# Optimization experiments

Measured on AMD Instinct MI355X. Metric: run time of the kernel, lower is better.

Reference implementation:

```python
import jax, jax.numpy as jnp
import numpy as np

GROUPS = 8
EPS = 1e-5


def group_norm(x, gamma, beta):
    b, c, h, w = x.shape
    xg = x.reshape(b, GROUPS, c // GROUPS, h, w)
    mu = jnp.mean(xg, axis=(2, 3, 4), keepdims=True)
    var = jnp.mean((xg - mu) ** 2, axis=(2, 3, 4), keepdims=True)
    xn = ((xg - mu) * jax.lax.rsqrt(var + EPS)).reshape(b, c, h, w)
    return xn * gamma[None, :, None, None] + beta[None, :, None, None]


def setup_inputs() -> dict:
    key = jax.random.key(0)
    ks = jax.random.split(key, 4)
    b, c, h, w = 4, 64, 64, 64
    x = jax.random.normal(ks[0], (b, c, h, w), dtype=jnp.float32)
    gamma = jnp.ones((c,), dtype=jnp.float32)
    beta = jnp.zeros((c,), dtype=jnp.float32)
    w_qkv = jax.random.normal(ks[1], (3 * c, c), dtype=jnp.float32) * (1.0 / np.sqrt(c))
    b_qkv = jnp.zeros((3 * c,), dtype=jnp.float32)
    w_proj = jax.random.normal(ks[2], (c, c), dtype=jnp.float32) * (1.0 / np.sqrt(c))
    b_proj = jnp.zeros((c,), dtype=jnp.float32)
    return {"x": x, "gamma": gamma, "beta": beta, "w_qkv": w_qkv,
            "b_qkv": b_qkv, "w_proj": w_proj, "b_proj": b_proj}


def reference(x, gamma, beta, w_qkv, b_qkv, w_proj, b_proj):
    b, c, h, w = x.shape
    xn = group_norm(x, gamma, beta)
    # 1x1 conv == per-pixel linear: [b,3c,h,w]
    qkv = jnp.einsum('oc,bchw->bohw', w_qkv, xn) + b_qkv[None, :, None, None]
    q, k, v = jnp.split(qkv, 3, axis=1)
    # flatten spatial -> tokens: [b, hw, c]
    def tok(t):
        return t.reshape(b, c, h * w).transpose(0, 2, 1)
    q, k, v = tok(q), tok(k), tok(v)
    scale = c ** (-0.5)
    attn = jnp.einsum('bqc,bkc->bqk', q, k) * scale  # [b, hw, hw]
    attn = jax.nn.softmax(attn, axis=-1)
    out = jnp.einsum('bqk,bkc->bqc', attn, v)  # [b, hw, c]
    out = out.transpose(0, 2, 1).reshape(b, c, h, w)
    out = jnp.einsum('oc,bchw->bohw', w_proj, out) + b_proj[None, :, None, None]
    return out + x
```

## Files before the change

kernel.cpp:

```cpp
#include <hip/hip_runtime.h>

typedef __bf16 bf16x8 __attribute__((ext_vector_type(8)));
typedef __bf16 bf16x4 __attribute__((ext_vector_type(4)));
typedef float  f32x4  __attribute__((ext_vector_type(4)));
typedef float  f32x16 __attribute__((ext_vector_type(16)));

#define GLD_LDS16(gsrc, ldst) \
  __builtin_amdgcn_global_load_lds((const __attribute__((address_space(1))) void*)(gsrc), \
                                   (__attribute__((address_space(3))) void*)(ldst), 16, 0, 0)

__device__ inline unsigned cvt_pk_bf16(float lo, float hi) {
  unsigned r;
  asm("v_cvt_pk_bf16_f32 %0, %1, %2" : "=v"(r) : "v"(lo), "v"(hi));
  return r;
}
__device__ inline void pl32_swap(unsigned& a, unsigned& b) {
  asm volatile("v_permlane32_swap_b32 %0, %1" : "+v"(a), "+v"(b));
}
__device__ inline f32x16 zero16() {
  f32x16 z;
#pragma unroll
  for (int i = 0; i < 16; ++i) z[i] = 0.f;
  return z;
}

__global__ __launch_bounds__(256) void gn_partial_k(const float* __restrict__ x,
                                                    float* __restrict__ partial) {
  __shared__ float red[2][4];
  const int t = threadIdx.x;
  const float4* base = (const float4*)(x + (size_t)blockIdx.x * 4096);
  float s = 0.f, sq = 0.f;
#pragma unroll
  for (int kk = 0; kk < 4; ++kk) {
    float4 v = base[t + kk * 256];
    s  += (v.x + v.y) + (v.z + v.w);
    sq += (v.x * v.x + v.y * v.y) + (v.z * v.z + v.w * v.w);
  }
#pragma unroll
  for (int o = 32; o >= 1; o >>= 1) {
    s  += __shfl_down(s, o, 64);
    sq += __shfl_down(sq, o, 64);
  }
  if ((t & 63) == 0) { red[0][t >> 6] = s; red[1][t >> 6] = sq; }
  __syncthreads();
  if (t == 0) {
    float S  = (red[0][0] + red[0][1]) + (red[0][2] + red[0][3]);
    float SQ = (red[1][0] + red[1][1]) + (red[1][2] + red[1][3]);
    partial[blockIdx.x * 2]     = S;
    partial[blockIdx.x * 2 + 1] = SQ;
  }
}

__global__ void gn_final_k(const float* __restrict__ partial, float* __restrict__ stats) {
  const int t = threadIdx.x;
  if (t < 32) {
    float S = 0.f, SQ = 0.f;
#pragma unroll
    for (int i = 0; i < 8; ++i) {
      S  += partial[(t * 8 + i) * 2];
      SQ += partial[(t * 8 + i) * 2 + 1];
    }
    float mean = S * (1.f / 32768.f);
    float var  = SQ * (1.f / 32768.f) - mean * mean;
    stats[t * 2]     = mean;
    stats[t * 2 + 1] = rsqrtf(fmaxf(var, 0.f) + 1e-5f);
  }
}

__global__ __launch_bounds__(192) void qkv_k(const float* __restrict__ x,
                                             const float* __restrict__ stats,
                                             const float* __restrict__ gamma,
                                             const float* __restrict__ beta,
                                             const float* __restrict__ w_qkv,
                                             const float* __restrict__ b_qkv,
                                             __bf16* __restrict__ qo,
                                             __bf16* __restrict__ ko,
                                             __bf16* __restrict__ vto) {
  __shared__ float xn_lds[32 * 68];
  __shared__ float v_lds[64 * 33];
  const int t  = threadIdx.x;
  const int b  = blockIdx.x >> 7;
  const int s0 = (blockIdx.x & 127) * 32;

  for (int idx = t; idx < 2048; idx += 192) {
    int c = idx >> 5, px = idx & 31;
    float v  = x[((size_t)(b * 64 + c)) * 4096 + s0 + px];
    int   g2 = (b * 8 + (c >> 3)) * 2;
    xn_lds[px * 68 + c] = (v - stats[g2]) * stats[g2 + 1] * gamma[c] + beta[c];
  }
  float4 wr[16];
  const float4* wrow = (const float4*)(w_qkv + t * 64);
#pragma unroll
  for (int i = 0; i < 16; ++i) wr[i] = wrow[i];
  const float bias = b_qkv[t];
  __syncthreads();

  for (int px = 0; px < 32; ++px) {
    const float4* xr = (const float4*)&xn_lds[px * 68];
    float a0 = bias, a1 = 0.f, a2 = 0.f, a3 = 0.f;
#pragma unroll
    for (int i = 0; i < 16; i += 4) {
      float4 x0 = xr[i], x1 = xr[i + 1], x2 = xr[i + 2], x3 = xr[i + 3];
      a0 += wr[i    ].x * x0.x + wr[i    ].y * x0.y + wr[i    ].z * x0.z + wr[i    ].w * x0.w;
      a1 += wr[i + 1].x * x1.x + wr[i + 1].y * x1.y + wr[i + 1].z * x1.z + wr[i + 1].w * x1.w;
      a2 += wr[i + 2].x * x2.x + wr[i + 2].y * x2.y + wr[i + 2].z * x2.z + wr[i + 2].w * x2.w;
      a3 += wr[i + 3].x * x3.x + wr[i + 3].y * x3.y + wr[i + 3].z * x3.z + wr[i + 3].w * x3.w;
    }
    float acc = (a0 + a1) + (a2 + a3);
    if (t < 64)
      qo[((size_t)b * 4096 + s0 + px) * 64 + t] = (__bf16)(acc * 0.18033688f);
    else if (t < 128)
      ko[((size_t)b * 4096 + s0 + px) * 64 + (t - 64)] = (__bf16)acc;
    else
      v_lds[(t - 128) * 33 + px] = acc;
  }
  __syncthreads();
  for (int u = t; u < 2048; u += 192) {
    int rowc = u >> 5, px = u & 31;
    vto[((size_t)(b * 64 + rowc)) * 4096 + s0 + px] = (__bf16)v_lds[rowc * 33 + px];
  }
}

__global__ __launch_bounds__(512, 2) void attn_k(const __bf16* __restrict__ q,
                                                 const __bf16* __restrict__ k,
                                                 const __bf16* __restrict__ vt,
                                                 __bf16* __restrict__ opart,
                                                 float* __restrict__ mlpart) {
  __shared__ __bf16 k_lds[3][4096];
  __shared__ __bf16 v_lds[3][4096];

  const int tid  = threadIdx.x;
  const int lane = tid & 63, w = tid >> 6;
  const int col  = lane & 31;
  const int h    = lane >> 5;
  const int swz  = col & 7;

  const int blk  = blockIdx.x;
  const int xcd  = blk & 7;
  const int b    = xcd >> 1;
  const int rest = blk >> 3;
  const int seg  = rest >> 3;
  const int qblk = (rest & 7) | ((xcd & 1) << 3);
  const int q0   = qblk * 256 + w * 32;
  const int j0b  = seg * 512;

  const __bf16* qp = q  + (size_t)b * 4096 * 64;
  const __bf16* kp = k  + (size_t)b * 4096 * 64;
  const __bf16* vp = vt + (size_t)b * 64 * 4096;

  bf16x8 qf[4];
#pragma unroll
  for (int kk = 0; kk < 4; ++kk)
    qf[kk] = *(const bf16x8*)(qp + (size_t)(q0 + col) * 64 + kk * 16 + h * 8);
  __builtin_amdgcn_sched_barrier(0);

  f32x16 acc0 = zero16(), acc1 = zero16();
  float m = -1e30f, l = 0.f;

  const int soff = tid * 16;
  const int sj = soff >> 7;
  const int sc = ((soff >> 4) & 7) ^ (sj & 7);

  auto stage = [&](int buf, int j0) {
    GLD_LDS16(kp + (size_t)(j0 + sj) * 64 + sc * 8, (char*)(&k_lds[buf][0]) + soff);
    GLD_LDS16(vp + (size_t)sj * 4096 + j0 + sc * 8, (char*)(&v_lds[buf][0]) + soff);
  };

  stage(0, j0b);
  stage(1, j0b + 64);

#pragma unroll
  for (int kt = 0; kt < 8; ++kt) {
    if (kt < 7) asm volatile("s_waitcnt vmcnt(2)" ::: "memory");
    else        asm volatile("s_waitcnt vmcnt(0)" ::: "memory");
    __builtin_amdgcn_s_barrier();

    if (kt < 6) stage((kt + 2) % 3, j0b + (kt + 2) * 64);

    const char* kbase = (const char*)&k_lds[kt % 3][0];
    const char* vbase = (const char*)&v_lds[kt % 3][0];

    f32x16 sa0 = zero16(), sa1 = zero16();
    __builtin_amdgcn_s_setprio(1);
#pragma unroll
    for (int kk = 0; kk < 4; ++kk) {
      bf16x8 kf0 = *(const bf16x8*)(kbase + col * 128        + (((2 * kk + h) ^ swz) << 4));
      bf16x8 kf1 = *(const bf16x8*)(kbase + (32 + col) * 128 + (((2 * kk + h) ^ swz) << 4));
      sa0 = __builtin_amdgcn_mfma_f32_32x32x16_bf16(kf0, qf[kk], sa0, 0, 0, 0);
      sa1 = __builtin_amdgcn_mfma_f32_32x32x16_bf16(kf1, qf[kk], sa1, 0, 0, 0);
    }
    __builtin_amdgcn_s_setprio(0);

    float x0 = fmaxf(fmaxf(sa0[0], sa0[1]),   fmaxf(sa0[2], sa0[3]));
    float x1 = fmaxf(fmaxf(sa0[4], sa0[5]),   fmaxf(sa0[6], sa0[7]));
    float x2 = fmaxf(fmaxf(sa0[8], sa0[9]),   fmaxf(sa0[10], sa0[11]));
    float x3 = fmaxf(fmaxf(sa0[12], sa0[13]), fmaxf(sa0[14], sa0[15]));
    float y0 = fmaxf(fmaxf(sa1[0], sa1[1]),   fmaxf(sa1[2], sa1[3]));
    float y1 = fmaxf(fmaxf(sa1[4], sa1[5]),   fmaxf(sa1[6], sa1[7]));
    float y2 = fmaxf(fmaxf(sa1[8], sa1[9]),   fmaxf(sa1[10], sa1[11]));
    float y3 = fmaxf(fmaxf(sa1[12], sa1[13]), fmaxf(sa1[14], sa1[15]));
    float mx = fmaxf(fmaxf(fmaxf(x0, x1), fmaxf(x2, x3)),
                     fmaxf(fmaxf(y0, y1), fmaxf(y2, y3)));
    mx = fmaxf(mx, __shfl_xor(mx, 32, 64));
    float mn = fmaxf(m, mx);
    float sf = exp2f(m - mn);
    m = mn;
    float ls = 0.f;
#pragma unroll
    for (int r = 0; r < 16; ++r) { sa0[r] = exp2f(sa0[r] - mn); ls += sa0[r]; }
#pragma unroll
    for (int r = 0; r < 16; ++r) { sa1[r] = exp2f(sa1[r] - mn); ls += sa1[r]; }
    l = l * sf + ls;
    acc0 *= sf;
    acc1 *= sf;

    unsigned w0[8], w1[8];
#pragma unroll
    for (int qd = 0; qd < 4; ++qd) {
      w0[qd * 2]     = cvt_pk_bf16(sa0[4 * qd],     sa0[4 * qd + 1]);
      w0[qd * 2 + 1] = cvt_pk_bf16(sa0[4 * qd + 2], sa0[4 * qd + 3]);
      w1[qd * 2]     = cvt_pk_bf16(sa1[4 * qd],     sa1[4 * qd + 1]);
      w1[qd * 2 + 1] = cvt_pk_bf16(sa1[4 * qd + 2], sa1[4 * qd + 3]);
    }
    bf16x8 pa[4];
#pragma unroll
    for (int c = 0; c < 4; ++c) {
      const unsigned* wt = (c < 2) ? w0 : w1;
      unsigned a0 = wt[(2 * (c & 1)) * 2],     b0 = wt[(2 * (c & 1) + 1) * 2];
      unsigned a1 = wt[(2 * (c & 1)) * 2 + 1], b1 = wt[(2 * (c & 1) + 1) * 2 + 1];
      pl32_swap(a0, b0);
      pl32_swap(a1, b1);
      uint4 u; u.x = a0; u.y = a1; u.z = b0; u.w = b1;
      pa[c] = __builtin_bit_cast(bf16x8, u);
    }

    __builtin_amdgcn_s_setprio(1);
#pragma unroll
    for (int c = 0; c < 4; ++c) {
      bf16x8 vf0 = *(const bf16x8*)(vbase + col * 128        + (((2 * c + h) ^ swz) << 4));
      bf16x8 vf1 = *(const bf16x8*)(vbase + (32 + col) * 128 + (((2 * c + h) ^ swz) << 4));
      acc0 = __builtin_amdgcn_mfma_f32_32x32x16_bf16(vf0, pa[c], acc0, 0, 0, 0);
      acc1 = __builtin_amdgcn_mfma_f32_32x32x16_bf16(vf1, pa[c], acc1, 0, 0, 0);
    }
    __builtin_amdgcn_s_setprio(0);
  }

  float lf = l + __shfl_xor(l, 32, 64);
  const int qrow = q0 + col;
  __bf16* ob = opart + ((size_t)(b * 8 + seg) * 4096 + qrow) * 64;
#pragma unroll
  for (int rq = 0; rq < 4; ++rq) {
    const int d0 = 8 * rq + 4 * h;
    bf16x4 o0 = {(__bf16)acc0[4 * rq], (__bf16)acc0[4 * rq + 1],
                 (__bf16)acc0[4 * rq + 2], (__bf16)acc0[4 * rq + 3]};
    bf16x4 o1 = {(__bf16)acc1[4 * rq], (__bf16)acc1[4 * rq + 1],
                 (__bf16)acc1[4 * rq + 2], (__bf16)acc1[4 * rq + 3]};
    *(bf16x4*)(ob + d0)      = o0;
    *(bf16x4*)(ob + 32 + d0) = o1;
  }
  if (h == 0) {
    float2 mlv; mlv.x = m; mlv.y = lf;
    *(float2*)(mlpart + ((size_t)(b * 8 + seg) * 4096 + qrow) * 2) = mlv;
  }
}

__global__ __launch_bounds__(256) void proj_k(const __bf16* __restrict__ opart,
                                              const float* __restrict__ mlpart,
                                              const float* __restrict__ x,
                                              const float* __restrict__ w_proj,
                                              const float* __restrict__ b_proj,
                                              float* __restrict__ out) {
  __shared__ float wseg[8][32];
  __shared__ float a_lds[32 * 68];
  __shared__ float o_lds[64 * 33];
  const int t  = threadIdx.x;
  const int b  = blockIdx.x >> 7;
  const int s0 = (blockIdx.x & 127) * 32;

  if (t < 32) {
    const int rowg = s0 + t;
    float ms[8], ls[8], es[8];
    float M = -1e30f;
#pragma unroll
    for (int s = 0; s < 8; ++s) {
      float2 ml = *(const float2*)(mlpart + ((size_t)(b * 8 + s) * 4096 + rowg) * 2);
      ms[s] = ml.x; ls[s] = ml.y;
      M = fmaxf(M, ms[s]);
    }
    float L = 0.f;
#pragma unroll
    for (int s = 0; s < 8; ++s) { es[s] = exp2f(ms[s] - M); L += es[s] * ls[s]; }
    float invL = 1.f / L;
#pragma unroll
    for (int s = 0; s < 8; ++s) wseg[s][t] = es[s] * invL;
  }
  __syncthreads();

  for (int i = t; i < 512; i += 256) {
    const int px = i >> 4, c4 = i & 15;
    const __bf16* obase = opart + ((size_t)(b * 8) * 4096 + s0 + px) * 64 + c4 * 4;
    float4 a = {0.f, 0.f, 0.f, 0.f};
#pragma unroll
    for (int s = 0; s < 8; ++s) {
      bf16x4 v = *(const bf16x4*)(obase + (size_t)s * 4096 * 64);
      float wv = wseg[s][px];
      a.x += wv * (float)v[0]; a.y += wv * (float)v[1];
      a.z += wv * (float)v[2]; a.w += wv * (float)v[3];
    }
    *(float4*)(&a_lds[px * 68 + c4 * 4]) = a;
  }

  const int o = t & 63, wg = t >> 6;
  float4 wr[16];
  const float4* wrow = (const float4*)(w_proj + o * 64);
#pragma unroll
  for (int i = 0; i < 16; ++i) wr[i] = wrow[i];
  const float bias = b_proj[o];
  __syncthreads();

  for (int pp = 0; pp < 8; ++pp) {
    const int px = wg * 8 + pp;
    const float4* ar = (const float4*)&a_lds[px * 68];
    float a0 = bias, a1 = 0.f, a2 = 0.f, a3 = 0.f;
#pragma unroll
    for (int i = 0; i < 16; i += 4) {
      float4 x0 = ar[i], x1 = ar[i + 1], x2 = ar[i + 2], x3 = ar[i + 3];
      a0 += wr[i    ].x * x0.x + wr[i    ].y * x0.y + wr[i    ].z * x0.z + wr[i    ].w * x0.w;
      a1 += wr[i + 1].x * x1.x + wr[i + 1].y * x1.y + wr[i + 1].z * x1.z + wr[i + 1].w * x1.w;
      a2 += wr[i + 2].x * x2.x + wr[i + 2].y * x2.y + wr[i + 2].z * x2.z + wr[i + 2].w * x2.w;
      a3 += wr[i + 3].x * x3.x + wr[i + 3].y * x3.y + wr[i + 3].z * x3.z + wr[i + 3].w * x3.w;
    }
    o_lds[o * 33 + px] = (a0 + a1) + (a2 + a3);
  }
  __syncthreads();
  for (int idx = t; idx < 2048; idx += 256) {
    const int c = idx >> 5, px = idx & 31;
    const size_t gi = ((size_t)(b * 64 + c)) * 4096 + s0 + px;
    out[gi] = o_lds[c * 33 + px] + x[gi];
  }
}

extern "C" void kernel_launch(void* const* d_in, const int* in_sizes, int n_in,
                              void* d_out, int out_size, void* d_ws, size_t ws_size,
                              hipStream_t stream) {
  const float* x      = (const float*)d_in[0];
  const float* gamma  = (const float*)d_in[1];
  const float* beta   = (const float*)d_in[2];
  const float* w_qkv  = (const float*)d_in[3];
  const float* b_qkv  = (const float*)d_in[4];
  const float* w_proj = (const float*)d_in[5];
  const float* b_proj = (const float*)d_in[6];
  float* out = (float*)d_out;

  char* ws = (char*)d_ws;
  float*  partial = (float*)ws;
  float*  stats   = partial + 512;
  __bf16* qb  = (__bf16*)(ws + 4096);
  __bf16* kb  = qb  + (size_t)4 * 4096 * 64;
  __bf16* vtb = kb  + (size_t)4 * 4096 * 64;
  __bf16* opart = vtb + (size_t)4 * 4096 * 64;
  float*  mlpart = (float*)(opart + (size_t)4 * 8 * 4096 * 64);

  gn_partial_k<<<256, 256, 0, stream>>>(x, partial);
  gn_final_k<<<1, 64, 0, stream>>>(partial, stats);
  qkv_k<<<512, 192, 0, stream>>>(x, stats, gamma, beta, w_qkv, b_qkv, qb, kb, vtb);
  attn_k<<<512, 512, 0, stream>>>(qb, kb, vtb, opart, mlpart);
  proj_k<<<512, 256, 0, stream>>>(opart, mlpart, x, w_proj, b_proj, out);
}
```

Measured before the change: 80.37 us.

## Compute QKV projection with split-bf16 MFMA and fold GroupNorm into scale/shift

```diff
diff --git a/kernel.cpp b/kernel.cpp
--- a/kernel.cpp
+++ b/kernel.cpp
@@ -25,9 +25,19 @@
 }
 
 __global__ __launch_bounds__(256) void gn_partial_k(const float* __restrict__ x,
-                                                    float* __restrict__ partial) {
+                                                    const float* __restrict__ w_qkv,
+                                                    float* __restrict__ partial,
+                                                    __bf16* __restrict__ whi,
+                                                    __bf16* __restrict__ wlo) {
   __shared__ float red[2][4];
   const int t = threadIdx.x;
+  if (blockIdx.x < 48) {
+    const int idx = blockIdx.x * 256 + t;
+    float wv = w_qkv[idx];
+    __bf16 hh = (__bf16)wv;
+    whi[idx] = hh;
+    wlo[idx] = (__bf16)(wv - (float)hh);
+  }
   const float4* base = (const float4*)(x + (size_t)blockIdx.x * 4096);
   float s = 0.f, sq = 0.f;
 #pragma unroll
@@ -51,8 +61,12 @@
   }
 }
 
-__global__ void gn_final_k(const float* __restrict__ partial, float* __restrict__ stats) {
+__global__ void gn_final_k(const float* __restrict__ partial,
+                           const float* __restrict__ gamma,
+                           const float* __restrict__ beta,
+                           float* __restrict__ sc) {
   const int t = threadIdx.x;
+  __shared__ float mu_s[32], rs_s[32];
   if (t < 32) {
     float S = 0.f, SQ = 0.f;
 #pragma unroll
@@ -62,62 +76,97 @@
     }
     float mean = S * (1.f / 32768.f);
     float var  = SQ * (1.f / 32768.f) - mean * mean;
-    stats[t * 2]     = mean;
-    stats[t * 2 + 1] = rsqrtf(fmaxf(var, 0.f) + 1e-5f);
-  }
-}
-
-__global__ __launch_bounds__(192) void qkv_k(const float* __restrict__ x,
-                                             const float* __restrict__ stats,
-                                             const float* __restrict__ gamma,
-                                             const float* __restrict__ beta,
-                                             const float* __restrict__ w_qkv,
+    mu_s[t] = mean;
+    rs_s[t] = rsqrtf(fmaxf(var, 0.f) + 1e-5f);
+  }
+  __syncthreads();
+  const int b = t >> 6, c = t & 63;
+  const int g = b * 8 + (c >> 3);
+  float scale = rs_s[g] * gamma[c];
+  sc[t * 2]     = scale;
+  sc[t * 2 + 1] = beta[c] - mu_s[g] * scale;
+}
+
+__global__ __launch_bounds__(256) void qkv_k(const float* __restrict__ x,
+                                             const float* __restrict__ sc,
+                                             const __bf16* __restrict__ whi,
+                                             const __bf16* __restrict__ wlo,
                                              const float* __restrict__ b_qkv,
                                              __bf16* __restrict__ qo,
                                              __bf16* __restrict__ ko,
                                              __bf16* __restrict__ vto) {
-  __shared__ float xn_lds[32 * 68];
-  __shared__ float v_lds[64 * 33];
-  const int t  = threadIdx.x;
-  const int b  = blockIdx.x >> 7;
-  const int s0 = (blockIdx.x & 127) * 32;
-
-  for (int idx = t; idx < 2048; idx += 192) {
-    int c = idx >> 5, px = idx & 31;
-    float v  = x[((size_t)(b * 64 + c)) * 4096 + s0 + px];
-    int   g2 = (b * 8 + (c >> 3)) * 2;
-    xn_lds[px * 68 + c] = (v - stats[g2]) * stats[g2 + 1] * gamma[c] + beta[c];
-  }
-  float4 wr[16];
-  const float4* wrow = (const float4*)(w_qkv + t * 64);
-#pragma unroll
-  for (int i = 0; i < 16; ++i) wr[i] = wrow[i];
-  const float bias = b_qkv[t];
-  __syncthreads();
-
-  for (int px = 0; px < 32; ++px) {
-    const float4* xr = (const float4*)&xn_lds[px * 68];
-    float a0 = bias, a1 = 0.f, a2 = 0.f, a3 = 0.f;
-#pragma unroll
-    for (int i = 0; i < 16; i += 4) {
-      float4 x0 = xr[i], x1 = xr[i + 1], x2 = xr[i + 2], x3 = xr[i + 3];
-      a0 += wr[i    ].x * x0.x + wr[i    ].y * x0.y + wr[i    ].z * x0.z + wr[i    ].w * x0.w;
-      a1 += wr[i + 1].x * x1.x + wr[i + 1].y * x1.y + wr[i + 1].z * x1.z + wr[i + 1].w * x1.w;
-      a2 += wr[i + 2].x * x2.x + wr[i + 2].y * x2.y + wr[i + 2].z * x2.z + wr[i + 2].w * x2.w;
-      a3 += wr[i + 3].x * x3.x + wr[i + 3].y * x3.y + wr[i + 3].z * x3.z + wr[i + 3].w * x3.w;
-    }
-    float acc = (a0 + a1) + (a2 + a3);
-    if (t < 64)
-      qo[((size_t)b * 4096 + s0 + px) * 64 + t] = (__bf16)(acc * 0.18033688f);
-    else if (t < 128)
-      ko[((size_t)b * 4096 + s0 + px) * 64 + (t - 64)] = (__bf16)acc;
-    else
-      v_lds[(t - 128) * 33 + px] = acc;
-  }
-  __syncthreads();
-  for (int u = t; u < 2048; u += 192) {
-    int rowc = u >> 5, px = u & 31;
-    vto[((size_t)(b * 64 + rowc)) * 4096 + s0 + px] = (__bf16)v_lds[rowc * 33 + px];
+  const int tid  = threadIdx.x;
+  const int lane = tid & 63, w = tid >> 6;
+  const int px16 = lane & 15, grp = lane >> 4;
+  const int b    = blockIdx.x >> 6;
+  const int s0   = (blockIdx.x & 63) * 64;
+  const int pxg  = s0 + w * 16 + px16;
+
+  bf16x8 bh[2], bl[2];
+#pragma unroll
+  for (int kk = 0; kk < 2; ++kk) {
+    bf16x8 hv, lv;
+#pragma unroll
+    for (int i = 0; i < 8; ++i) {
+      const int c = kk * 32 + grp * 8 + i;
+      float xv = x[((size_t)(b * 64 + c) * 4096) + pxg];
+      float2 s = *(const float2*)(sc + (b * 64 + c) * 2);
+      float xn = fmaf(xv, s.x, s.y);
+      __bf16 hh = (__bf16)xn;
+      hv[i] = hh;
+      lv[i] = (__bf16)(xn - (float)hh);
+    }
+    bh[kk] = hv;
+    bl[kk] = lv;
+  }
+
+  f32x4 acc[12];
+#pragma unroll
+  for (int ot = 0; ot < 12; ++ot) {
+    const int o = ot * 16 + px16;
+    f32x4 a = {0.f, 0.f, 0.f, 0.f};
+#pragma unroll
+    for (int kk = 0; kk < 2; ++kk) {
+      const size_t wo = (size_t)o * 64 + kk * 32 + grp * 8;
+      bf16x8 ah = *(const bf16x8*)(whi + wo);
+      bf16x8 al = *(const bf16x8*)(wlo + wo);
+      a = __builtin_amdgcn_mfma_f32_16x16x32_bf16(ah, bh[kk], a, 0, 0, 0);
+      a = __builtin_amdgcn_mfma_f32_16x16x32_bf16(ah, bl[kk], a, 0, 0, 0);
+      a = __builtin_amdgcn_mfma_f32_16x16x32_bf16(al, bh[kk], a, 0, 0, 0);
+    }
+    acc[ot] = a;
+  }
+
+#pragma unroll
+  for (int ot = 0; ot < 4; ++ot) {
+    const int ob = ot * 16 + grp * 4;
+    float4 bias = *(const float4*)(b_qkv + ob);
+    f32x4 a = acc[ot];
+    bf16x4 qv = {(__bf16)((a[0] + bias.x) * 0.18033688f),
+                 (__bf16)((a[1] + bias.y) * 0.18033688f),
+                 (__bf16)((a[2] + bias.z) * 0.18033688f),
+                 (__bf16)((a[3] + bias.w) * 0.18033688f)};
+    *(bf16x4*)(qo + ((size_t)b * 4096 + pxg) * 64 + ob) = qv;
+  }
+#pragma unroll
+  for (int ot = 4; ot < 8; ++ot) {
+    const int ob = (ot - 4) * 16 + grp * 4;
+    float4 bias = *(const float4*)(b_qkv + 64 + ob);
+    f32x4 a = acc[ot];
+    bf16x4 kv = {(__bf16)(a[0] + bias.x), (__bf16)(a[1] + bias.y),
+                 (__bf16)(a[2] + bias.z), (__bf16)(a[3] + bias.w)};
+    *(bf16x4*)(ko + ((size_t)b * 4096 + pxg) * 64 + ob) = kv;
+  }
+#pragma unroll
+  for (int ot = 8; ot < 12; ++ot) {
+    const int ob = (ot - 8) * 16 + grp * 4;
+    float4 bias = *(const float4*)(b_qkv + 128 + ob);
+    f32x4 a = acc[ot];
+#pragma unroll
+    for (int r = 0; r < 4; ++r) {
+      float bv = (r == 0) ? bias.x : (r == 1) ? bias.y : (r == 2) ? bias.z : bias.w;
+      vto[((size_t)(b * 64 + ob + r)) * 4096 + pxg] = (__bf16)(a[r] + bv);
+    }
   }
 }
 
@@ -159,11 +208,11 @@
 
   const int soff = tid * 16;
   const int sj = soff >> 7;
-  const int sc = ((soff >> 4) & 7) ^ (sj & 7);
+  const int sc2 = ((soff >> 4) & 7) ^ (sj & 7);
 
   auto stage = [&](int buf, int j0) {
-    GLD_LDS16(kp + (size_t)(j0 + sj) * 64 + sc * 8, (char*)(&k_lds[buf][0]) + soff);
-    GLD_LDS16(vp + (size_t)sj * 4096 + j0 + sc * 8, (char*)(&v_lds[buf][0]) + soff);
+    GLD_LDS16(kp + (size_t)(j0 + sj) * 64 + sc2 * 8, (char*)(&k_lds[buf][0]) + soff);
+    GLD_LDS16(vp + (size_t)sj * 4096 + j0 + sc2 * 8, (char*)(&v_lds[buf][0]) + soff);
   };
 
   stage(0, j0b);
@@ -354,16 +403,18 @@
 
   char* ws = (char*)d_ws;
   float*  partial = (float*)ws;
-  float*  stats   = partial + 512;
-  __bf16* qb  = (__bf16*)(ws + 4096);
+  float*  scbuf   = partial + 512;
+  __bf16* whi     = (__bf16*)(ws + 4096);
+  __bf16* wlo     = whi + 12288;
+  __bf16* qb  = (__bf16*)(ws + 65536);
   __bf16* kb  = qb  + (size_t)4 * 4096 * 64;
   __bf16* vtb = kb  + (size_t)4 * 4096 * 64;
   __bf16* opart = vtb + (size_t)4 * 4096 * 64;
   float*  mlpart = (float*)(opart + (size_t)4 * 8 * 4096 * 64);
 
-  gn_partial_k<<<256, 256, 0, stream>>>(x, partial);
-  gn_final_k<<<1, 64, 0, stream>>>(partial, stats);
-  qkv_k<<<512, 192, 0, stream>>>(x, stats, gamma, beta, w_qkv, b_qkv, qb, kb, vtb);
+  gn_partial_k<<<256, 256, 0, stream>>>(x, w_qkv, partial, whi, wlo);
+  gn_final_k<<<1, 256, 0, stream>>>(partial, gamma, beta, scbuf);
+  qkv_k<<<256, 256, 0, stream>>>(x, scbuf, whi, wlo, b_qkv, qb, kb, vtb);
   attn_k<<<512, 512, 0, stream>>>(qb, kb, vtb, opart, mlpart);
   proj_k<<<512, 256, 0, stream>>>(opart, mlpart, x, w_proj, b_proj, out);
 }
```

After: 71.53 us. 11.0% less time.
